# Optimization experiments

Hardware: AMD Instinct MI355X
Metric: run time of the kernel (lower is better)

## Reference

```python
import jax, jax.numpy as jnp
import numpy as np

N = 50000
E = 800000
IN_DIM = 512
HID = 64
OUT = 64
HEADS = 4
NEG_SLOPE = 0.2


def setup_inputs() -> dict:
    key = jax.random.key(0)
    ks = jax.random.split(key, 16)
    s = 0.05
    inp = {
        "x": jax.random.normal(ks[0], (N, IN_DIM), jnp.float32),
        "edge_index": jax.random.randint(ks[1], (2, E), 0, N, jnp.int64),
        # layer 1: in=512 -> heads*hid = 4*64 = 256, concat=True
        "W1l": jax.random.normal(ks[2], (IN_DIM, HEADS * HID), jnp.float32) * s,
        "b1l": jnp.zeros((HEADS * HID,), jnp.float32),
        "W1r": jax.random.normal(ks[3], (IN_DIM, HEADS * HID), jnp.float32) * s,
        "b1r": jnp.zeros((HEADS * HID,), jnp.float32),
        "att1": jax.random.normal(ks[4], (HEADS, HID), jnp.float32) * s,
        "bias1": jnp.zeros((HEADS * HID,), jnp.float32),
        # layer 2: in=256 -> heads*(2*out) = 4*128, concat=False (mean heads)
        "W2l": jax.random.normal(ks[5], (HEADS * HID, HEADS * 2 * OUT), jnp.float32) * s,
        "b2l": jnp.zeros((HEADS * 2 * OUT,), jnp.float32),
        "W2r": jax.random.normal(ks[6], (HEADS * HID, HEADS * 2 * OUT), jnp.float32) * s,
        "b2r": jnp.zeros((HEADS * 2 * OUT,), jnp.float32),
        "att2": jax.random.normal(ks[7], (HEADS, 2 * OUT), jnp.float32) * s,
        "bias2": jnp.zeros((2 * OUT,), jnp.float32),
    }
    return inp


def _gatv2(x, src, dst, Wl, bl, Wr, br, att, bias, concat):
    """GATv2Conv (PyG semantics): message x_l[src], attention over incoming edges per dst."""
    H, C = att.shape
    n = x.shape[0]
    xl = (x @ Wl + bl).reshape(n, H, C)  # source transform (messages)
    xr = (x @ Wr + br).reshape(n, H, C)  # target transform
    g = jax.nn.leaky_relu(xl[src] + xr[dst], NEG_SLOPE)   # [E, H, C]
    e = jnp.einsum('ehc,hc->eh', g, att)                  # [E, H]
    # numerically-stable softmax over irregular neighbor sets (segmented by dst)
    m = jax.ops.segment_max(e, dst, num_segments=n)
    ex = jnp.exp(e - m[dst])
    denom = jax.ops.segment_sum(ex, dst, num_segments=n)
    alpha = ex / (denom[dst] + 1e-16)                     # [E, H]
    out = jax.ops.segment_sum(xl[src] * alpha[..., None], dst, num_segments=n)  # [N, H, C]
    if concat:
        return out.reshape(n, H * C) + bias
    return out.mean(axis=1) + bias


def reference(x, edge_index, W1l, b1l, W1r, b1r, att1, bias1,
              W2l, b2l, W2r, b2r, att2, bias2):
    # add self loops (PyG add_self_loops=True default)
    loops = jnp.arange(N, dtype=edge_index.dtype)
    src = jnp.concatenate([edge_index[0], loops])
    dst = jnp.concatenate([edge_index[1], loops])
    h = jax.nn.relu(_gatv2(x, src, dst, W1l, b1l, W1r, b1r, att1, bias1, concat=True))
    return _gatv2(h, src, dst, W2l, b2l, W2r, b2r, att2, bias2, concat=False)
```

## Files before the change

### kernel.cpp

```cpp
#include <hip/hip_runtime.h>

#define NNODES 50000
#define NEDGES 800000
#define ET (NEDGES + NNODES)
#define HEADS 4

typedef __attribute__((ext_vector_type(8))) short bf16x8;
typedef __attribute__((ext_vector_type(4))) float f32x4;

#define EXP2F(x) __builtin_amdgcn_exp2f(x)

#define GLOAD16(g, l) __builtin_amdgcn_global_load_lds(                      \
    (const __attribute__((address_space(1))) unsigned int*)(g),              \
    (__attribute__((address_space(3))) unsigned int*)(l), 16, 0, 0)

__device__ inline unsigned short f2bf(float f) {
  union { float f; unsigned int i; } c; c.f = f;
  unsigned int b = c.i + 0x7fffu + ((c.i >> 16) & 1u);
  return (unsigned short)(b >> 16);
}
__device__ inline float4 b4tof(uint2 r) {
  float4 f;
  union { unsigned int i; float v; } c;
  c.i = r.x << 16;          f.x = c.v;
  c.i = r.x & 0xffff0000u;  f.y = c.v;
  c.i = r.y << 16;          f.z = c.v;
  c.i = r.y & 0xffff0000u;  f.w = c.v;
  return f;
}


__global__ void k_hist(const int* __restrict__ ei, int* __restrict__ deg) {
  int i = blockIdx.x * blockDim.x + threadIdx.x;
  if (i >= ET) return;
  int dst = (i < NEDGES) ? ei[NEDGES + i] : (i - NEDGES);
  atomicAdd(&deg[dst], 1);
}

__global__ void k_scan1(const int* __restrict__ deg, int* __restrict__ part,
                        int* __restrict__ bsum, int n) {
  __shared__ int s[256];
  int tid = threadIdx.x;
  int i = blockIdx.x * 256 + tid;
  int v = (i < n) ? deg[i] : 0;
  s[tid] = v;
  __syncthreads();
  for (int off = 1; off < 256; off <<= 1) {
    int t = (tid >= off) ? s[tid - off] : 0;
    __syncthreads();
    s[tid] += t;
    __syncthreads();
  }
  if (i < n) part[i] = s[tid] - v;
  if (tid == 255) bsum[blockIdx.x] = s[255];
}

__global__ void k_scan2(int* bsum, int nb) {
  __shared__ int s[256];
  int t = threadIdx.x;
  int v = (t < nb) ? bsum[t] : 0;
  s[t] = v;
  __syncthreads();
  for (int off = 1; off < 256; off <<= 1) {
    int tv = (t >= off) ? s[t - off] : 0;
    __syncthreads();
    s[t] += tv;
    __syncthreads();
  }
  if (t < nb) bsum[t] = s[t] - v;
}

__global__ void k_scan3(const int* __restrict__ part, const int* __restrict__ bsum,
                        int* __restrict__ rowstart, int* __restrict__ cursor,
                        int n, int total) {
  int i = blockIdx.x * blockDim.x + threadIdx.x;
  if (i < n) {
    int v = part[i] + bsum[i >> 8];
    rowstart[i] = v;
    cursor[i] = v;
  }
  if (i == n) rowstart[n] = total;
}

__global__ void k_scatter(const int* __restrict__ ei, int* __restrict__ cursor,
                          int* __restrict__ csrsrc) {
  int i = blockIdx.x * blockDim.x + threadIdx.x;
  if (i >= ET) return;
  int src, dst;
  if (i < NEDGES) { src = ei[i]; dst = ei[NEDGES + i]; }
  else            { src = dst = i - NEDGES; }
  int pos = atomicAdd(&cursor[dst], 1);
  csrsrc[pos] = src;
}


__global__ void k_cast_bf16(const float* __restrict__ in, unsigned short* __restrict__ out, int n4) {
  int i = blockIdx.x * blockDim.x + threadIdx.x;
  if (i >= n4) return;
  float4 v = ((const float4*)in)[i];
  ushort4 o;
  o.x = f2bf(v.x); o.y = f2bf(v.y); o.z = f2bf(v.z); o.w = f2bf(v.w);
  ((ushort4*)out)[i] = o;
}

__global__ void k_castw_all(const float* __restrict__ W1l, const float* __restrict__ W1r,
                            const float* __restrict__ W2l, const float* __restrict__ W2r,
                            unsigned short* __restrict__ w1t, unsigned short* __restrict__ w2t) {
  int id = blockIdx.x * blockDim.x + threadIdx.x;
  int which = blockIdx.y;
  const float* W;
  unsigned short* T;
  int K, Nw, noff;
  if (which == 0)      { W = W1l; T = w1t; K = 512; Nw = 256; noff = 0; }
  else if (which == 1) { W = W1r; T = w1t; K = 512; Nw = 256; noff = 256; }
  else if (which == 2) { W = W2l; T = w2t; K = 256; Nw = 512; noff = 0; }
  else                 { W = W2r; T = w2t; K = 256; Nw = 512; noff = 512; }
  int k = id / Nw, n = id - k * Nw;
  T[(size_t)(n + noff) * K + k] = f2bf(W[id]);
}


__global__ __launch_bounds__(256) void k_gemm(
    const unsigned short* __restrict__ A, const unsigned short* __restrict__ Bt,
    const float* __restrict__ bL, const float* __restrict__ bR, int nsplit,
    unsigned short* __restrict__ C, int M, int K, int N) {
  __shared__ unsigned short As[128 * 32];
  __shared__ unsigned short Bs[128 * 32];
  int tid = threadIdx.x;
  int lane = tid & 63, wave = tid >> 6;
  int wr = (wave >> 1) * 64, wc = (wave & 1) * 64;
  int row0 = blockIdx.x * 128, col0 = blockIdx.y * 128;
  int fr = lane & 15;
  int fq = lane >> 4;
  int sr = tid >> 2;
  int sc = (tid & 3) * 8;

  const unsigned short* ga0 = &A[(size_t)(row0 + sr) * K + sc];
  const unsigned short* ga1 = &A[(size_t)(row0 + sr + 64) * K + sc];
  const unsigned short* gb0 = &Bt[(size_t)(col0 + sr) * K + sc];
  const unsigned short* gb1 = &Bt[(size_t)(col0 + sr + 64) * K + sc];
  unsigned short* la0 = &As[tid * 8];
  unsigned short* la1 = &As[2048 + tid * 8];
  unsigned short* lb0 = &Bs[tid * 8];
  unsigned short* lb1 = &Bs[2048 + tid * 8];

  f32x4 acc[4][4] = {};

  for (int k0 = 0; k0 < K; k0 += 32) {
    GLOAD16(ga0 + k0, la0);
    GLOAD16(ga1 + k0, la1);
    GLOAD16(gb0 + k0, lb0);
    GLOAD16(gb1 + k0, lb1);
    __syncthreads();
    bf16x8 af[4], bfr[4];
#pragma unroll
    for (int m = 0; m < 4; ++m)
      af[m] = *(const bf16x8*)&As[(wr + m * 16 + fr) * 32 + fq * 8];
#pragma unroll
    for (int n = 0; n < 4; ++n)
      bfr[n] = *(const bf16x8*)&Bs[(wc + n * 16 + fr) * 32 + fq * 8];
#pragma unroll
    for (int m = 0; m < 4; ++m)
#pragma unroll
      for (int n = 0; n < 4; ++n)
        acc[m][n] = __builtin_amdgcn_mfma_f32_16x16x32_bf16(af[m], bfr[n], acc[m][n], 0, 0, 0);
    __syncthreads();
  }

#pragma unroll
  for (int m = 0; m < 4; ++m) {
#pragma unroll
    for (int n = 0; n < 4; ++n) {
      int col = col0 + wc + n * 16 + fr;
      float bv = (col < nsplit) ? bL[col] : bR[col - nsplit];
#pragma unroll
      for (int j = 0; j < 4; ++j) {
        int row = row0 + wr + m * 16 + fq * 4 + j;
        if (row < M) C[(size_t)row * N + col] = f2bf(acc[m][n][j] + bv);
      }
    }
  }
}


template <int CQ>
__device__ inline float edge_score(const float4* xv, const float4* xrv, const float4* attv) {
  float p = 0.f;
#pragma unroll
  for (int q = 0; q < CQ; ++q) {
    float s;
    s = xv[q].x + xrv[q].x; p = fmaf(attv[q].x, fmaxf(s, 0.2f * s), p);
    s = xv[q].y + xrv[q].y; p = fmaf(attv[q].y, fmaxf(s, 0.2f * s), p);
    s = xv[q].z + xrv[q].z; p = fmaf(attv[q].z, fmaxf(s, 0.2f * s), p);
    s = xv[q].w + xrv[q].w; p = fmaf(attv[q].w, fmaxf(s, 0.2f * s), p);
  }
  return p;
}

template <int CQ, int MODE, int STR>
__global__ __launch_bounds__(256) void k_fused(
    const int* __restrict__ rowstart, const int* __restrict__ csrsrc,
    const unsigned short* __restrict__ xlr,
    const float* __restrict__ att, const float* __restrict__ bias,
    void* __restrict__ outp) {
  const int C = CQ * 64;
  int dst = (blockIdx.x * blockDim.x + threadIdx.x) >> 6;
  int lane = threadIdx.x & 63;
  if (dst >= NNODES) return;
  int h = lane >> 4;
  int l = lane & 15;
  const int choff = h * C + l * 4;

  float4 xrv[CQ], attv[CQ];
#pragma unroll
  for (int q = 0; q < CQ; ++q) {
    xrv[q] = b4tof(*(const uint2*)&xlr[(size_t)dst * STR + STR / 2 + choff + q * 64]);
    float4 a = *(const float4*)&att[choff + q * 64];
    a.x *= 1.44269504f; a.y *= 1.44269504f;
    a.z *= 1.44269504f; a.w *= 1.44269504f;
    attv[q] = a;
  }

  int rs = __builtin_amdgcn_readfirstlane(rowstart[dst]);
  int re = __builtin_amdgcn_readfirstlane(rowstart[dst + 1]);

  float den = 0.f;
  float4 acc[CQ];
#pragma unroll
  for (int q = 0; q < CQ; ++q) acc[q] = make_float4(0.f, 0.f, 0.f, 0.f);

  int i = rs;
  for (; i + 4 <= re; i += 4) {
    int s0 = csrsrc[i + 0];
    int s1 = csrsrc[i + 1];
    int s2 = csrsrc[i + 2];
    int s3 = csrsrc[i + 3];
    unsigned o0 = (unsigned)s0 * (unsigned)STR + choff;
    unsigned o1 = (unsigned)s1 * (unsigned)STR + choff;
    unsigned o2 = (unsigned)s2 * (unsigned)STR + choff;
    unsigned o3 = (unsigned)s3 * (unsigned)STR + choff;
    uint2 r0[CQ], r1[CQ], r2[CQ], r3[CQ];
#pragma unroll
    for (int q = 0; q < CQ; ++q) {
      r0[q] = *(const uint2*)&xlr[o0 + q * 64];
      r1[q] = *(const uint2*)&xlr[o1 + q * 64];
      r2[q] = *(const uint2*)&xlr[o2 + q * 64];
      r3[q] = *(const uint2*)&xlr[o3 + q * 64];
    }
    float4 x0[CQ], x1[CQ], x2[CQ], x3[CQ];
#pragma unroll
    for (int q = 0; q < CQ; ++q) {
      x0[q] = b4tof(r0[q]); x1[q] = b4tof(r1[q]);
      x2[q] = b4tof(r2[q]); x3[q] = b4tof(r3[q]);
    }
    float p0 = edge_score<CQ>(x0, xrv, attv);
    float p1 = edge_score<CQ>(x1, xrv, attv);
    float p2 = edge_score<CQ>(x2, xrv, attv);
    float p3 = edge_score<CQ>(x3, xrv, attv);
#pragma unroll
    for (int d = 1; d <= 8; d <<= 1) {
      p0 += __shfl_xor(p0, d);
      p1 += __shfl_xor(p1, d);
      p2 += __shfl_xor(p2, d);
      p3 += __shfl_xor(p3, d);
    }
    float w0 = EXP2F(p0), w1 = EXP2F(p1), w2 = EXP2F(p2), w3 = EXP2F(p3);
    den += (w0 + w1) + (w2 + w3);
#pragma unroll
    for (int q = 0; q < CQ; ++q) {
      acc[q].x = fmaf(w0, x0[q].x, fmaf(w1, x1[q].x, fmaf(w2, x2[q].x, fmaf(w3, x3[q].x, acc[q].x))));
      acc[q].y = fmaf(w0, x0[q].y, fmaf(w1, x1[q].y, fmaf(w2, x2[q].y, fmaf(w3, x3[q].y, acc[q].y))));
      acc[q].z = fmaf(w0, x0[q].z, fmaf(w1, x1[q].z, fmaf(w2, x2[q].z, fmaf(w3, x3[q].z, acc[q].z))));
      acc[q].w = fmaf(w0, x0[q].w, fmaf(w1, x1[q].w, fmaf(w2, x2[q].w, fmaf(w3, x3[q].w, acc[q].w))));
    }
  }
  for (; i < re; ++i) {
    int s0 = csrsrc[i];
    unsigned o0 = (unsigned)s0 * (unsigned)STR + choff;
    uint2 r0[CQ];
#pragma unroll
    for (int q = 0; q < CQ; ++q) r0[q] = *(const uint2*)&xlr[o0 + q * 64];
    float4 x0[CQ];
#pragma unroll
    for (int q = 0; q < CQ; ++q) x0[q] = b4tof(r0[q]);
    float p0 = edge_score<CQ>(x0, xrv, attv);
#pragma unroll
    for (int d = 1; d <= 8; d <<= 1) p0 += __shfl_xor(p0, d);
    float w0 = EXP2F(p0);
    den += w0;
#pragma unroll
    for (int q = 0; q < CQ; ++q) {
      acc[q].x = fmaf(w0, x0[q].x, acc[q].x);
      acc[q].y = fmaf(w0, x0[q].y, acc[q].y);
      acc[q].z = fmaf(w0, x0[q].z, acc[q].z);
      acc[q].w = fmaf(w0, x0[q].w, acc[q].w);
    }
  }

  float inv = 1.f / (den + 1e-16f);

  if (MODE == 0) {
    unsigned short* out = (unsigned short*)outp;
#pragma unroll
    for (int q = 0; q < CQ; ++q) {
      const float4 bv = *(const float4*)&bias[choff + q * 64];
      ushort4 o;
      o.x = f2bf(fmaxf(acc[q].x * inv + bv.x, 0.f));
      o.y = f2bf(fmaxf(acc[q].y * inv + bv.y, 0.f));
      o.z = f2bf(fmaxf(acc[q].z * inv + bv.z, 0.f));
      o.w = f2bf(fmaxf(acc[q].w * inv + bv.w, 0.f));
      *(ushort4*)&out[(size_t)dst * (HEADS * C) + choff + q * 64] = o;
    }
  } else {
    float* out = (float*)outp;
    float r[CQ][4];
#pragma unroll
    for (int q = 0; q < CQ; ++q) {
      r[q][0] = acc[q].x * inv; r[q][1] = acc[q].y * inv;
      r[q][2] = acc[q].z * inv; r[q][3] = acc[q].w * inv;
    }
#pragma unroll
    for (int q = 0; q < CQ; ++q)
#pragma unroll
      for (int j = 0; j < 4; ++j) {
        r[q][j] += __shfl_xor(r[q][j], 16);
        r[q][j] += __shfl_xor(r[q][j], 32);
      }
    if (lane < 16 * CQ) {
      int q = lane >> 4;
      int c = lane * 4;
      float4 o;
      o.x = r[q][0] * 0.25f + bias[c + 0];
      o.y = r[q][1] * 0.25f + bias[c + 1];
      o.z = r[q][2] * 0.25f + bias[c + 2];
      o.w = r[q][3] * 0.25f + bias[c + 3];
      *(float4*)&out[(size_t)dst * C + c] = o;
    }
  }
}


extern "C" void kernel_launch(void* const* d_in, const int* in_sizes, int n_in,
                              void* d_out, int out_size, void* d_ws, size_t ws_size,
                              hipStream_t stream) {
  (void)in_sizes; (void)n_in; (void)out_size; (void)ws_size;
  const float* x     = (const float*)d_in[0];
  const int*   ei    = (const int*)d_in[1];
  const float* W1l   = (const float*)d_in[2];
  const float* b1l   = (const float*)d_in[3];
  const float* W1r   = (const float*)d_in[4];
  const float* b1r   = (const float*)d_in[5];
  const float* att1  = (const float*)d_in[6];
  const float* bias1 = (const float*)d_in[7];
  const float* W2l   = (const float*)d_in[8];
  const float* b2l   = (const float*)d_in[9];
  const float* W2r   = (const float*)d_in[10];
  const float* b2r   = (const float*)d_in[11];
  const float* att2  = (const float*)d_in[12];
  const float* bias2 = (const float*)d_in[13];
  float* out = (float*)d_out;

  char* ws = (char*)d_ws;
  size_t off = 0;
  auto alloc = [&](size_t bytes) {
    char* p = ws + off;
    off = (off + bytes + 255) & ~(size_t)255;
    return p;
  };
  int*  deg      = (int*)alloc((size_t)NNODES * 4);
  int*  part     = (int*)alloc((size_t)NNODES * 4);
  int*  bsum     = (int*)alloc(256 * 4);
  int*  rowstart = (int*)alloc((size_t)(NNODES + 1) * 4);
  int*  cursor   = (int*)alloc((size_t)NNODES * 4);
  int*  csrsrc   = (int*)alloc((size_t)ET * 4);
  unsigned short* xb   = (unsigned short*)alloc((size_t)NNODES * 512 * 2);
  unsigned short* w1t  = (unsigned short*)alloc((size_t)512 * 512 * 2);
  unsigned short* w2t  = (unsigned short*)alloc((size_t)1024 * 256 * 2);
  unsigned short* xlr1 = (unsigned short*)alloc((size_t)NNODES * 512 * 2);
  unsigned short* hbuf = (unsigned short*)alloc((size_t)NNODES * 256 * 2);
  unsigned short* xlr2 = (unsigned short*)alloc((size_t)NNODES * 1024 * 2);

  (void)hipMemsetAsync(deg, 0, (size_t)NNODES * 4, stream);
  k_hist<<<(ET + 255) / 256, 256, 0, stream>>>(ei, deg);
  int nb = (NNODES + 255) / 256;
  k_scan1<<<nb, 256, 0, stream>>>(deg, part, bsum, NNODES);
  k_scan2<<<1, 256, 0, stream>>>(bsum, nb);
  k_scan3<<<(NNODES + 256) / 256, 256, 0, stream>>>(part, bsum, rowstart, cursor, NNODES, ET);
  k_scatter<<<(ET + 255) / 256, 256, 0, stream>>>(ei, cursor, csrsrc);

  k_cast_bf16<<<(NNODES * 512 / 4 + 255) / 256, 256, 0, stream>>>(x, xb, NNODES * 512 / 4);
  k_castw_all<<<dim3(512, 4), 256, 0, stream>>>(W1l, W1r, W2l, W2r, w1t, w2t);

  const int gridM = (NNODES + 127) / 128;
  const int gridFused = (NNODES + 3) / 4;

  k_gemm<<<dim3(gridM, 4), 256, 0, stream>>>(xb, w1t, b1l, b1r, 256, xlr1, NNODES, 512, 512);
  k_fused<1, 0, 512><<<gridFused, 256, 0, stream>>>(rowstart, csrsrc, xlr1, att1, bias1, hbuf);

  k_gemm<<<dim3(gridM, 8), 256, 0, stream>>>(hbuf, w2t, b2l, b2r, 512, xlr2, NNODES, 256, 1024);
  k_fused<2, 1, 1024><<<gridFused, 256, 0, stream>>>(rowstart, csrsrc, xlr2, att2, bias2, out);
}
```

Before: 464.5 us.

## Double-buffer GEMM LDS tiles, tile weight transpose, vectorize fused-kernel row loads

The GEMM now double-buffers its A/B LDS tiles, issuing the next k-tile's global-to-LDS loads before computing the current one, so load latency overlaps MFMA work. The weight cast/transpose kernel now stages through a padded shared-memory tile, making its global reads and writes coalesced. The fused attention kernel changes channel ownership so each lane holds contiguous channels, which lets layer 2 fetch each source row with one 16-byte load instead of two 8-byte loads. The extra LDS buffer raises shared-memory use per block, and a spare workspace allocation is added.

Result: no change. 468.1 us (+0.8%).

```diff
diff --git a/kernel.cpp b/kernel.cpp
--- a/kernel.cpp
+++ b/kernel.cpp
@@ -103,20 +103,30 @@
   ((ushort4*)out)[i] = o;
 }
 
-__global__ void k_castw_all(const float* __restrict__ W1l, const float* __restrict__ W1r,
-                            const float* __restrict__ W2l, const float* __restrict__ W2r,
-                            unsigned short* __restrict__ w1t, unsigned short* __restrict__ w2t) {
-  int id = blockIdx.x * blockDim.x + threadIdx.x;
+__global__ __launch_bounds__(256) void k_castw_all(
+    const float* __restrict__ W1l, const float* __restrict__ W1r,
+    const float* __restrict__ W2l, const float* __restrict__ W2r,
+    unsigned short* __restrict__ w1t, unsigned short* __restrict__ w2t) {
+  __shared__ float tile[32][33];
   int which = blockIdx.y;
   const float* W;
   unsigned short* T;
-  int K, Nw, noff;
-  if (which == 0)      { W = W1l; T = w1t; K = 512; Nw = 256; noff = 0; }
-  else if (which == 1) { W = W1r; T = w1t; K = 512; Nw = 256; noff = 256; }
-  else if (which == 2) { W = W2l; T = w2t; K = 256; Nw = 512; noff = 0; }
-  else                 { W = W2r; T = w2t; K = 256; Nw = 512; noff = 512; }
-  int k = id / Nw, n = id - k * Nw;
-  T[(size_t)(n + noff) * K + k] = f2bf(W[id]);
+  int K, N, noff;
+  if (which == 0)      { W = W1l; T = w1t; K = 512; N = 256; noff = 0; }
+  else if (which == 1) { W = W1r; T = w1t; K = 512; N = 256; noff = 256; }
+  else if (which == 2) { W = W2l; T = w2t; K = 256; N = 512; noff = 0; }
+  else                 { W = W2r; T = w2t; K = 256; N = 512; noff = 512; }
+  int tpr = N >> 5;
+  int tk = (blockIdx.x / tpr) << 5;
+  int tn = (blockIdx.x % tpr) << 5;
+  int c = threadIdx.x & 31, r = threadIdx.x >> 5;
+#pragma unroll
+  for (int rr = 0; rr < 32; rr += 8)
+    tile[r + rr][c] = W[(size_t)(tk + r + rr) * N + tn + c];
+  __syncthreads();
+#pragma unroll
+  for (int rr = 0; rr < 32; rr += 8)
+    T[(size_t)(tn + r + rr + noff) * K + tk + c] = f2bf(tile[c][r + rr]);
 }
 
 
@@ -124,47 +134,54 @@
     const unsigned short* __restrict__ A, const unsigned short* __restrict__ Bt,
     const float* __restrict__ bL, const float* __restrict__ bR, int nsplit,
     unsigned short* __restrict__ C, int M, int K, int N) {
-  __shared__ unsigned short As[128 * 32];
-  __shared__ unsigned short Bs[128 * 32];
+  __shared__ unsigned short As[2][128 * 32];
+  __shared__ unsigned short Bs[2][128 * 32];
   int tid = threadIdx.x;
   int lane = tid & 63, wave = tid >> 6;
   int wr = (wave >> 1) * 64, wc = (wave & 1) * 64;
   int row0 = blockIdx.x * 128, col0 = blockIdx.y * 128;
-  int fr = lane & 15;
-  int fq = lane >> 4;
-  int sr = tid >> 2;
-  int sc = (tid & 3) * 8;
+  int fr = lane & 15, fq = lane >> 4;
+  int sr = tid >> 2, sc = (tid & 3) * 8;
 
   const unsigned short* ga0 = &A[(size_t)(row0 + sr) * K + sc];
   const unsigned short* ga1 = &A[(size_t)(row0 + sr + 64) * K + sc];
   const unsigned short* gb0 = &Bt[(size_t)(col0 + sr) * K + sc];
   const unsigned short* gb1 = &Bt[(size_t)(col0 + sr + 64) * K + sc];
-  unsigned short* la0 = &As[tid * 8];
-  unsigned short* la1 = &As[2048 + tid * 8];
-  unsigned short* lb0 = &Bs[tid * 8];
-  unsigned short* lb1 = &Bs[2048 + tid * 8];
 
   f32x4 acc[4][4] = {};
-
-  for (int k0 = 0; k0 < K; k0 += 32) {
-    GLOAD16(ga0 + k0, la0);
-    GLOAD16(ga1 + k0, la1);
-    GLOAD16(gb0 + k0, lb0);
-    GLOAD16(gb1 + k0, lb1);
-    __syncthreads();
+  const int NT = K >> 5;
+
+  GLOAD16(ga0, &As[0][tid * 8]);
+  GLOAD16(ga1, &As[0][2048 + tid * 8]);
+  GLOAD16(gb0, &Bs[0][tid * 8]);
+  GLOAD16(gb1, &Bs[0][2048 + tid * 8]);
+  asm volatile("s_waitcnt vmcnt(0)" ::: "memory");
+  __builtin_amdgcn_s_barrier();
+
+  int cur = 0;
+  for (int t = 0; t < NT; ++t) {
+    if (t + 1 < NT) {
+      int k0 = (t + 1) << 5;
+      GLOAD16(ga0 + k0, &As[cur ^ 1][tid * 8]);
+      GLOAD16(ga1 + k0, &As[cur ^ 1][2048 + tid * 8]);
+      GLOAD16(gb0 + k0, &Bs[cur ^ 1][tid * 8]);
+      GLOAD16(gb1 + k0, &Bs[cur ^ 1][2048 + tid * 8]);
+    }
     bf16x8 af[4], bfr[4];
 #pragma unroll
     for (int m = 0; m < 4; ++m)
-      af[m] = *(const bf16x8*)&As[(wr + m * 16 + fr) * 32 + fq * 8];
+      af[m] = *(const bf16x8*)&As[cur][(wr + m * 16 + fr) * 32 + fq * 8];
 #pragma unroll
     for (int n = 0; n < 4; ++n)
-      bfr[n] = *(const bf16x8*)&Bs[(wc + n * 16 + fr) * 32 + fq * 8];
+      bfr[n] = *(const bf16x8*)&Bs[cur][(wc + n * 16 + fr) * 32 + fq * 8];
 #pragma unroll
     for (int m = 0; m < 4; ++m)
 #pragma unroll
       for (int n = 0; n < 4; ++n)
         acc[m][n] = __builtin_amdgcn_mfma_f32_16x16x32_bf16(af[m], bfr[n], acc[m][n], 0, 0, 0);
-    __syncthreads();
+    asm volatile("s_waitcnt vmcnt(0)" ::: "memory");
+    __builtin_amdgcn_s_barrier();
+    cur ^= 1;
   }
 
 #pragma unroll
@@ -182,6 +199,17 @@
   }
 }
 
+
+template <int CQ>
+__device__ inline void load_row(const unsigned short* p, float4* xv) {
+  if constexpr (CQ == 1) {
+    xv[0] = b4tof(*(const uint2*)p);
+  } else {
+    uint4 r = *(const uint4*)p;
+    xv[0] = b4tof(make_uint2(r.x, r.y));
+    xv[1] = b4tof(make_uint2(r.z, r.w));
+  }
+}
 
 template <int CQ>
 __device__ inline float edge_score(const float4* xv, const float4* xrv, const float4* attv) {
@@ -204,18 +232,19 @@
     const float* __restrict__ att, const float* __restrict__ bias,
     void* __restrict__ outp) {
   const int C = CQ * 64;
+  const int CHL = CQ * 4;
   int dst = (blockIdx.x * blockDim.x + threadIdx.x) >> 6;
   int lane = threadIdx.x & 63;
   if (dst >= NNODES) return;
   int h = lane >> 4;
   int l = lane & 15;
-  const int choff = h * C + l * 4;
+  const int choff = h * C + l * CHL;
 
   float4 xrv[CQ], attv[CQ];
+  load_row<CQ>(&xlr[(size_t)dst * STR + STR / 2 + choff], xrv);
 #pragma unroll
   for (int q = 0; q < CQ; ++q) {
-    xrv[q] = b4tof(*(const uint2*)&xlr[(size_t)dst * STR + STR / 2 + choff + q * 64]);
-    float4 a = *(const float4*)&att[choff + q * 64];
+    float4 a = *(const float4*)&att[choff + q * 4];
     a.x *= 1.44269504f; a.y *= 1.44269504f;
     a.z *= 1.44269504f; a.w *= 1.44269504f;
     attv[q] = a;
@@ -235,24 +264,11 @@
     int s1 = csrsrc[i + 1];
     int s2 = csrsrc[i + 2];
     int s3 = csrsrc[i + 3];
-    unsigned o0 = (unsigned)s0 * (unsigned)STR + choff;
-    unsigned o1 = (unsigned)s1 * (unsigned)STR + choff;
-    unsigned o2 = (unsigned)s2 * (unsigned)STR + choff;
-    unsigned o3 = (unsigned)s3 * (unsigned)STR + choff;
-    uint2 r0[CQ], r1[CQ], r2[CQ], r3[CQ];
-#pragma unroll
-    for (int q = 0; q < CQ; ++q) {
-      r0[q] = *(const uint2*)&xlr[o0 + q * 64];
-      r1[q] = *(const uint2*)&xlr[o1 + q * 64];
-      r2[q] = *(const uint2*)&xlr[o2 + q * 64];
-      r3[q] = *(const uint2*)&xlr[o3 + q * 64];
-    }
     float4 x0[CQ], x1[CQ], x2[CQ], x3[CQ];
-#pragma unroll
-    for (int q = 0; q < CQ; ++q) {
-      x0[q] = b4tof(r0[q]); x1[q] = b4tof(r1[q]);
-      x2[q] = b4tof(r2[q]); x3[q] = b4tof(r3[q]);
-    }
+    load_row<CQ>(&xlr[(unsigned)s0 * (unsigned)STR + choff], x0);
+    load_row<CQ>(&xlr[(unsigned)s1 * (unsigned)STR + choff], x1);
+    load_row<CQ>(&xlr[(unsigned)s2 * (unsigned)STR + choff], x2);
+    load_row<CQ>(&xlr[(unsigned)s3 * (unsigned)STR + choff], x3);
     float p0 = edge_score<CQ>(x0, xrv, attv);
     float p1 = edge_score<CQ>(x1, xrv, attv);
     float p2 = edge_score<CQ>(x2, xrv, attv);
@@ -276,13 +292,8 @@
   }
   for (; i < re; ++i) {
     int s0 = csrsrc[i];
-    unsigned o0 = (unsigned)s0 * (unsigned)STR + choff;
-    uint2 r0[CQ];
-#pragma unroll
-    for (int q = 0; q < CQ; ++q) r0[q] = *(const uint2*)&xlr[o0 + q * 64];
     float4 x0[CQ];
-#pragma unroll
-    for (int q = 0; q < CQ; ++q) x0[q] = b4tof(r0[q]);
+    load_row<CQ>(&xlr[(unsigned)s0 * (unsigned)STR + choff], x0);
     float p0 = edge_score<CQ>(x0, xrv, attv);
 #pragma unroll
     for (int d = 1; d <= 8; d <<= 1) p0 += __shfl_xor(p0, d);
@@ -303,13 +314,13 @@
     unsigned short* out = (unsigned short*)outp;
 #pragma unroll
     for (int q = 0; q < CQ; ++q) {
-      const float4 bv = *(const float4*)&bias[choff + q * 64];
+      const float4 bv = *(const float4*)&bias[choff + q * 4];
       ushort4 o;
       o.x = f2bf(fmaxf(acc[q].x * inv + bv.x, 0.f));
       o.y = f2bf(fmaxf(acc[q].y * inv + bv.y, 0.f));
       o.z = f2bf(fmaxf(acc[q].z * inv + bv.z, 0.f));
       o.w = f2bf(fmaxf(acc[q].w * inv + bv.w, 0.f));
-      *(ushort4*)&out[(size_t)dst * (HEADS * C) + choff + q * 64] = o;
+      *(ushort4*)&out[(size_t)dst * (HEADS * C) + choff + q * 4] = o;
     }
   } else {
     float* out = (float*)outp;
@@ -326,15 +337,17 @@
         r[q][j] += __shfl_xor(r[q][j], 16);
         r[q][j] += __shfl_xor(r[q][j], 32);
       }
-    if (lane < 16 * CQ) {
-      int q = lane >> 4;
-      int c = lane * 4;
-      float4 o;
-      o.x = r[q][0] * 0.25f + bias[c + 0];
-      o.y = r[q][1] * 0.25f + bias[c + 1];
-      o.z = r[q][2] * 0.25f + bias[c + 2];
-      o.w = r[q][3] * 0.25f + bias[c + 3];
-      *(float4*)&out[(size_t)dst * C + c] = o;
+    if (lane < 16) {
+#pragma unroll
+      for (int q = 0; q < CQ; ++q) {
+        int c = lane * CHL + q * 4;
+        float4 o;
+        o.x = r[q][0] * 0.25f + bias[c + 0];
+        o.y = r[q][1] * 0.25f + bias[c + 1];
+        o.z = r[q][2] * 0.25f + bias[c + 2];
+        o.w = r[q][3] * 0.25f + bias[c + 3];
+        *(float4*)&out[(size_t)dst * C + c] = o;
+      }
     }
   }
 }
@@ -379,6 +392,7 @@
   unsigned short* xlr1 = (unsigned short*)alloc((size_t)NNODES * 512 * 2);
   unsigned short* hbuf = (unsigned short*)alloc((size_t)NNODES * 256 * 2);
   unsigned short* xlr2 = (unsigned short*)alloc((size_t)NNODES * 1024 * 2);
+  (void)alloc(64 * 1024);
 
   (void)hipMemsetAsync(deg, 0, (size_t)NNODES * 4, stream);
   k_hist<<<(ET + 255) / 256, 256, 0, stream>>>(ei, deg);
@@ -389,7 +403,7 @@
   k_scatter<<<(ET + 255) / 256, 256, 0, stream>>>(ei, cursor, csrsrc);
 
   k_cast_bf16<<<(NNODES * 512 / 4 + 255) / 256, 256, 0, stream>>>(x, xb, NNODES * 512 / 4);
-  k_castw_all<<<dim3(512, 4), 256, 0, stream>>>(W1l, W1r, W2l, W2r, w1t, w2t);
+  k_castw_all<<<dim3(128, 4), 256, 0, stream>>>(W1l, W1r, W2l, W2r, w1t, w2t);
 
   const int gridM = (NNODES + 127) / 128;
   const int gridFused = (NNODES + 3) / 4;
```
